# Optimization experiments

Measured on AMD Instinct MI355X. Metric: run time of the kernel, lower is better.

Reference implementation:

```python
import jax, jax.numpy as jnp
import numpy as np

NQ = 12  # num_qubits
NL = 4   # num_layers (StronglyEntanglingLayers depth)
BATCH = 512


def _rx(a):
    # RX(a) = [[cos(a/2), -i sin(a/2)], [-i sin(a/2), cos(a/2)]]; a: (...,) float -> (...,2,2) complex64
    c = jnp.cos(a / 2)
    s = jnp.sin(a / 2)
    return jnp.stack([jnp.stack([c + 0j, -1j * s], -1),
                      jnp.stack([-1j * s, c + 0j], -1)], -2)


def _rot(phi, theta, omega):
    # Pennylane Rot(phi,theta,omega) = RZ(omega) RY(theta) RZ(phi)
    ct = jnp.cos(theta / 2)
    st = jnp.sin(theta / 2)
    ep = jnp.exp(-0.5j * (phi + omega))   # e^{-i(phi+omega)/2}
    em = jnp.exp(-0.5j * (phi - omega))   # e^{-i(phi-omega)/2}
    return jnp.stack([jnp.stack([ep * ct, -jnp.conj(em) * st], -1),
                      jnp.stack([em * st, jnp.conj(ep) * ct], -1)], -2)


def _apply_1q_shared(state, U, q):
    # state: (B,) + (2,)*n; U: (2,2) shared across batch
    s = jnp.moveaxis(state, q + 1, -1)
    s = s @ U.T
    return jnp.moveaxis(s, -1, q + 1)


def _apply_1q_batched(state, U, q):
    # U: (B,2,2), one gate per batch element (AngleEmbedding)
    s = jnp.moveaxis(state, q + 1, -1)
    s = jnp.einsum('b...i,bij->b...j', s, U)
    return jnp.moveaxis(s, -1, q + 1)


def _apply_cnot(state, c, t):
    # flip target axis on the control=1 slice
    s = jnp.moveaxis(state, (c + 1, t + 1), (1, 2))  # (B,2,2,rest)
    s = jnp.stack([s[:, 0], s[:, 1, ::-1]], axis=1)
    return jnp.moveaxis(s, (1, 2), (c + 1, t + 1))


def _circuit(batch_inputs, weights):
    B, n = batch_inputs.shape
    state = jnp.zeros((B, 2 ** n), jnp.complex64).at[:, 0].set(1.0)
    state = state.reshape((B,) + (2,) * n)
    # AngleEmbedding: RX(x_i) on wire i
    Ux = _rx(batch_inputs)  # (B,n,2,2)
    for q in range(n):
        state = _apply_1q_batched(state, Ux[:, q], q)
    # StronglyEntanglingLayers: per layer Rot on each wire then CNOT ring with range r
    Ur = _rot(weights[..., 0], weights[..., 1], weights[..., 2])  # (L,n,2,2)
    for l in range(NL):
        for q in range(n):
            state = _apply_1q_shared(state, Ur[l, q], q)
        r = (l % (n - 1)) + 1  # pennylane default ranges
        for q in range(n):
            state = _apply_cnot(state, q, (q + r) % n)
    # <Z_q> = p(0 on q) - p(1 on q)
    probs = state.real ** 2 + state.imag ** 2
    zs = []
    for q in range(n):
        p = jnp.moveaxis(probs, q + 1, 1).reshape(B, 2, -1).sum(-1)
        zs.append(p[:, 0] - p[:, 1])
    return jnp.stack(zs, axis=1)  # (B,n) float32


def setup_inputs() -> dict:
    key = jax.random.key(0)
    k1, k2, k3, k4 = jax.random.split(key, 4)
    return {
        'batch_inputs': jax.random.normal(k1, (BATCH, NQ), dtype=jnp.float32),
        'weights': jax.random.normal(k2, (NL, NQ, 3), dtype=jnp.float32),
        'head_w': jax.random.normal(k3, (1, NQ), dtype=jnp.float32) / np.sqrt(NQ),
        'head_b': jax.random.normal(k4, (1,), dtype=jnp.float32),
    }


def reference(batch_inputs, weights, head_w, head_b):
    expvals = _circuit(batch_inputs, weights)      # (B, NQ)
    return (expvals @ head_w.T + head_b)[:, 0]     # (B,)
```

## Files before the change

kernel.cpp:

```cpp
#include <hip/hip_runtime.h>

#define NQ 12
#define NL 4
#define NT 256

typedef float f32x2 __attribute__((ext_vector_type(2)));

constexpr unsigned sidx_c(unsigned x) { return x ^ ((x >> 4) & 15u) ^ ((x >> 8) & 15u); }

constexpr unsigned gmap_inv(int l, unsigned v) {
    int r = l + 1; unsigned x = v;
    for (int q = 0; q < NQ; ++q) {
        int cb = NQ - 1 - q, tw = (q + r) % NQ, tb = NQ - 1 - tw;
        x ^= ((x >> cb) & 1u) << tb;
    }
    return x;
}

struct Tabs {
    unsigned lcol[3][8];
    unsigned scol[3][16];
    unsigned rfin[NQ];
};
constexpr Tabs make_tabs() {
    Tabs T{};
    for (int l = 0; l < 3; ++l) {
        unsigned colb[12];
        for (int bit = 0; bit < 12; ++bit) colb[bit] = sidx_c(gmap_inv(l, 1u << bit)) << 3;
        for (int j = 0; j < 6; ++j) T.lcol[l][j] = colb[4 + j];
        T.lcol[l][6] = colb[10];
        T.lcol[l][7] = colb[11];
        for (int s = 0; s < 16; ++s) {
            unsigned v = 0;
            for (int bp = 0; bp < 4; ++bp) if ((s >> bp) & 1) v ^= colb[bp];
            T.scol[l][s] = v;
        }
    }
    for (int q = 0; q < NQ; ++q) {
        const int bpos = 11 - q;
        unsigned m = 0;
        for (int j = 0; j < 12; ++j)
            m |= ((gmap_inv(3, 1u << j) >> bpos) & 1u) << j;
        T.rfin[q] = m;
    }
    return T;
}
__constant__ Tabs TB = make_tabs();
constexpr Tabs CT = make_tabs();

template<int CTRL>
__device__ __forceinline__ f32x2 dpp2(f32x2 v) {
    f32x2 r;
    r.x = __int_as_float(__builtin_amdgcn_update_dpp(__float_as_int(v.x), __float_as_int(v.x), CTRL, 0xF, 0xF, false));
    r.y = __int_as_float(__builtin_amdgcn_update_dpp(__float_as_int(v.y), __float_as_int(v.y), CTRL, 0xF, 0xF, false));
    return r;
}
__device__ __forceinline__ void pswap32(f32x2 v, f32x2& lo, f32x2& hi) {
    float ax = v.x, bx = v.x;
    asm("v_permlane32_swap_b32 %0, %1" : "+v"(ax), "+v"(bx));
    float ay = v.y, by = v.y;
    asm("v_permlane32_swap_b32 %0, %1" : "+v"(ay), "+v"(by));
    lo = f32x2{ax, ay}; hi = f32x2{bx, by};
}
__device__ __forceinline__ void pswap16(f32x2 v, f32x2& ev, f32x2& od) {
    float ax = v.x, bx = v.x;
    asm("v_permlane16_swap_b32 %0, %1" : "+v"(ax), "+v"(bx));
    float ay = v.y, by = v.y;
    asm("v_permlane16_swap_b32 %0, %1" : "+v"(ay), "+v"(by));
    ev = f32x2{ax, ay}; od = f32x2{bx, by};
}

__device__ __forceinline__ void gates2to11(f32x2 rp[8], f32x2 ip[8], const float (*gmL)[8], int lane) {
    {
        const float4 ga = *(const float4*)&gmL[2][0];
        const float4 gb = *(const float4*)&gmL[2][4];
        const int h = (lane >> 5) & 1;
        const float car = h ? gb.x : ga.x, cai = h ? gb.y : ga.y;
        const float cbr = h ? gb.z : ga.z, cbi = h ? gb.w : ga.w;
        #pragma unroll
        for (int k = 0; k < 8; ++k) {
            f32x2 r0r, r1r, r0i, r1i;
            pswap32(rp[k], r0r, r1r);
            pswap32(ip[k], r0i, r1i);
            rp[k] = car*r0r - cai*r0i + cbr*r1r - cbi*r1i;
            ip[k] = cai*r0r + car*r0i + cbi*r1r + cbr*r1i;
        }
    }
    {
        const float4 ga = *(const float4*)&gmL[3][0];
        const float4 gb = *(const float4*)&gmL[3][4];
        const int h = (lane >> 4) & 1;
        const float car = h ? gb.x : ga.x, cai = h ? gb.y : ga.y;
        const float cbr = h ? gb.z : ga.z, cbi = h ? gb.w : ga.w;
        #pragma unroll
        for (int k = 0; k < 8; ++k) {
            f32x2 r0r, r1r, r0i, r1i;
            pswap16(rp[k], r0r, r1r);
            pswap16(ip[k], r0i, r1i);
            rp[k] = car*r0r - cai*r0i + cbr*r1r - cbi*r1i;
            ip[k] = cai*r0r + car*r0i + cbi*r1r + cbr*r1i;
        }
    }
    {
        const float4 ga = *(const float4*)&gmL[4][0];
        const float4 gb = *(const float4*)&gmL[4][4];
        const int h = (lane >> 3) & 1;
        const float cMer = h ? gb.z : ga.x, cMei = h ? gb.w : ga.y;
        const float cOtr = h ? gb.x : ga.z, cOti = h ? gb.y : ga.w;
        #pragma unroll
        for (int k = 0; k < 8; ++k) {
            const f32x2 pR = dpp2<0x128>(rp[k]), pI = dpp2<0x128>(ip[k]);
            const f32x2 nr = cMer*rp[k] - cMei*ip[k] + cOtr*pR - cOti*pI;
            const f32x2 ni = cMei*rp[k] + cMer*ip[k] + cOti*pR + cOtr*pI;
            rp[k] = nr; ip[k] = ni;
        }
    }
    {
        const float4 ga = *(const float4*)&gmL[5][0];
        const float4 gb = *(const float4*)&gmL[5][4];
        const int h = (lane >> 2) & 1;
        const float cMer = h ? gb.z : ga.x, cMei = h ? gb.w : ga.y;
        const float cOtr = h ? gb.x : ga.z, cOti = h ? gb.y : ga.w;
        #pragma unroll
        for (int k = 0; k < 8; ++k) {
            const f32x2 pR = dpp2<0xB1>(dpp2<0x4E>(dpp2<0x141>(rp[k])));
            const f32x2 pI = dpp2<0xB1>(dpp2<0x4E>(dpp2<0x141>(ip[k])));
            const f32x2 nr = cMer*rp[k] - cMei*ip[k] + cOtr*pR - cOti*pI;
            const f32x2 ni = cMei*rp[k] + cMer*ip[k] + cOti*pR + cOtr*pI;
            rp[k] = nr; ip[k] = ni;
        }
    }
    {
        const float4 ga = *(const float4*)&gmL[6][0];
        const float4 gb = *(const float4*)&gmL[6][4];
        const int h = (lane >> 1) & 1;
        const float cMer = h ? gb.z : ga.x, cMei = h ? gb.w : ga.y;
        const float cOtr = h ? gb.x : ga.z, cOti = h ? gb.y : ga.w;
        #pragma unroll
        for (int k = 0; k < 8; ++k) {
            const f32x2 pR = dpp2<0x4E>(rp[k]), pI = dpp2<0x4E>(ip[k]);
            const f32x2 nr = cMer*rp[k] - cMei*ip[k] + cOtr*pR - cOti*pI;
            const f32x2 ni = cMei*rp[k] + cMer*ip[k] + cOti*pR + cOtr*pI;
            rp[k] = nr; ip[k] = ni;
        }
    }
    {
        const float4 ga = *(const float4*)&gmL[7][0];
        const float4 gb = *(const float4*)&gmL[7][4];
        const int h = lane & 1;
        const float cMer = h ? gb.z : ga.x, cMei = h ? gb.w : ga.y;
        const float cOtr = h ? gb.x : ga.z, cOti = h ? gb.y : ga.w;
        #pragma unroll
        for (int k = 0; k < 8; ++k) {
            const f32x2 pR = dpp2<0xB1>(rp[k]), pI = dpp2<0xB1>(ip[k]);
            const f32x2 nr = cMer*rp[k] - cMei*ip[k] + cOtr*pR - cOti*pI;
            const f32x2 ni = cMei*rp[k] + cMer*ip[k] + cOti*pR + cOtr*pI;
            rp[k] = nr; ip[k] = ni;
        }
    }
    #pragma unroll
    for (int wq = 8; wq <= 10; ++wq) {
        const int rb2 = 10 - wq;
        const float4 ga = *(const float4*)&gmL[wq][0];
        const float4 gb = *(const float4*)&gmL[wq][4];
        #pragma unroll
        for (int h2 = 0; h2 < 4; ++h2) {
            const int k0 = ((h2 >> rb2) << (rb2 + 1)) | (h2 & ((1 << rb2) - 1));
            const int k1 = k0 | (1 << rb2);
            const f32x2 a0r = rp[k0], a0i = ip[k0], a1r = rp[k1], a1i = ip[k1];
            rp[k0] = ga.x*a0r - ga.y*a0i + ga.z*a1r - ga.w*a1i;
            ip[k0] = ga.y*a0r + ga.x*a0i + ga.w*a1r + ga.z*a1i;
            rp[k1] = gb.x*a0r - gb.y*a0i + gb.z*a1r - gb.w*a1i;
            ip[k1] = gb.y*a0r + gb.x*a0i + gb.w*a1r + gb.z*a1i;
        }
    }
    {
        const float4 ga = *(const float4*)&gmL[11][0];
        const float4 gb = *(const float4*)&gmL[11][4];
        const f32x2 K0r = f32x2{ga.x, gb.x}, K0i = f32x2{ga.y, gb.y};
        const f32x2 K1r = f32x2{ga.z, gb.z}, K1i = f32x2{ga.w, gb.w};
        #pragma unroll
        for (int k = 0; k < 8; ++k) {
            const float a0r = rp[k].x, a0i = ip[k].x, a1r = rp[k].y, a1i = ip[k].y;
            rp[k] = K0r*a0r - K0i*a0i + K1r*a1r - K1i*a1i;
            ip[k] = K0i*a0r + K0r*a0i + K1i*a1r + K1r*a1i;
        }
    }
}

__device__ __forceinline__ void read_w01(f32x2 rp[8], f32x2 ip[8], const float2* st, unsigned wbyte,
                                         const float (*gmL)[8], int b11, int b10) {
    const float4 ga0 = *(const float4*)&gmL[0][0];
    const float4 gb0 = *(const float4*)&gmL[0][4];
    const float4 ga1 = *(const float4*)&gmL[1][0];
    const float4 gb1 = *(const float4*)&gmL[1][4];
    const float d0r = b11 ? gb0.z : ga0.x, d0i = b11 ? gb0.w : ga0.y;
    const float o0r = b11 ? gb0.x : ga0.z, o0i = b11 ? gb0.y : ga0.w;
    const float d1r = b10 ? gb1.z : ga1.x, d1i = b10 ? gb1.w : ga1.y;
    const float o1r = b10 ? gb1.x : ga1.z, o1i = b10 ? gb1.y : ga1.w;
    const float dwr  = d0r*d1r - d0i*d1i, dwi  = d0r*d1i + d0i*d1r;
    const float dp1r = o0r*d1r - o0i*d1i, dp1i = o0r*d1i + o0i*d1r;
    const float dp2r = d0r*o1r - d0i*o1i, dp2i = d0r*o1i + d0i*o1r;
    const float dp3r = o0r*o1r - o0i*o1i, dp3i = o0r*o1i + o0i*o1r;
    #pragma unroll
    for (int k = 0; k < 8; ++k) {
        const unsigned a0 = wbyte ^ ((unsigned)(2 * k) << 3);
        const unsigned a1 = a0 ^ 8u;
        const float2 o_0 = *(const float2*)((const char*)st + a0);
        const float2 o_1 = *(const float2*)((const char*)st + a1);
        const float2 v_0 = *(const float2*)((const char*)st + (a0 ^ 0x2020u));
        const float2 v_1 = *(const float2*)((const char*)st + (a1 ^ 0x2020u));
        const float2 u_0 = *(const float2*)((const char*)st + (a0 ^ 0x4040u));
        const float2 u_1 = *(const float2*)((const char*)st + (a1 ^ 0x4040u));
        const float2 w_0 = *(const float2*)((const char*)st + (a0 ^ 0x6060u));
        const float2 w_1 = *(const float2*)((const char*)st + (a1 ^ 0x6060u));
        const f32x2 orr = f32x2{o_0.x, o_1.x}, oii = f32x2{o_0.y, o_1.y};
        const f32x2 p2r = f32x2{v_0.x, v_1.x}, p2i = f32x2{v_0.y, v_1.y};
        const f32x2 p1r = f32x2{u_0.x, u_1.x}, p1i = f32x2{u_0.y, u_1.y};
        const f32x2 p3r = f32x2{w_0.x, w_1.x}, p3i = f32x2{w_0.y, w_1.y};
        rp[k] = dwr*orr - dwi*oii + dp1r*p1r - dp1i*p1i + dp2r*p2r - dp2i*p2i + dp3r*p3r - dp3i*p3i;
        ip[k] = dwi*orr + dwr*oii + dp1i*p1r + dp1r*p1i + dp2i*p2r + dp2r*p2i + dp3i*p3r + dp3r*p3i;
    }
}

__device__ __forceinline__ void scatter_l(const f32x2 rp[8], const f32x2 ip[8], float2* st,
                                          int l, int lane, int b10, int b11) {
    unsigned sbase = 0;
    #pragma unroll
    for (int j = 0; j < 6; ++j) if ((lane >> j) & 1) sbase ^= TB.lcol[l][j];
    if (b10) sbase ^= TB.lcol[l][6];
    if (b11) sbase ^= TB.lcol[l][7];
    #pragma unroll
    for (int k = 0; k < 8; ++k) {
        *(float2*)((char*)st + (sbase ^ TB.scol[l][2 * k]))     = make_float2(rp[k].x, ip[k].x);
        *(float2*)((char*)st + (sbase ^ TB.scol[l][2 * k + 1])) = make_float2(rp[k].y, ip[k].y);
    }
}

__global__ __launch_bounds__(NT) void qsim_kernel(
    const float* __restrict__ xin,
    const float* __restrict__ wts,
    const float* __restrict__ hw,
    const float* __restrict__ hb,
    float* __restrict__ out)
{
    __shared__ float2 st[4096];
    __shared__ float  gm[NL * NQ][8];
    __shared__ float  wred[4];

    const int tid  = threadIdx.x;
    const int lane = tid & 63;
    const int wv   = tid >> 6;
    const int b    = blockIdx.x;
    const int b11  = wv >> 1, b10 = wv & 1;

    if (tid < NL * NQ) {
        const float phi = wts[tid * 3 + 0];
        const float th  = wts[tid * 3 + 1];
        const float om  = wts[tid * 3 + 2];
        const float ct  = cosf(0.5f * th), stt = sinf(0.5f * th);
        const float apo = -0.5f * (phi + om), amo = -0.5f * (phi - om);
        const float epr = cosf(apo), epi = sinf(apo);
        const float emr = cosf(amo), emi = sinf(amo);
        float* g = gm[tid];
        g[0] =  epr * ct;  g[1] =  epi * ct;
        g[2] = -emr * stt; g[3] =  emi * stt;
        g[4] =  emr * stt; g[5] =  emi * stt;
        g[6] =  epr * ct;  g[7] = -epi * ct;
    }

    float cv[NQ], sv[NQ];
    #pragma unroll
    for (int bp = 0; bp < NQ; ++bp) {
        const float a = 0.5f * xin[b * NQ + (NQ - 1 - bp)];
        cv[bp] = __cosf(a); sv[bp] = __sinf(a);
    }
    float MS[16];
    MS[0] = cv[0]; MS[1] = sv[0];
    #pragma unroll
    for (int bit = 1; bit < 4; ++bit) {
        #pragma unroll
        for (int j = (1 << bit) - 1; j >= 0; --j) {
            MS[j | (1 << bit)] = MS[j] * sv[bit];
            MS[j]              = MS[j] * cv[bit];
        }
    }

    const unsigned xbase = ((unsigned)wv << 10) | ((unsigned)lane << 4);
    const unsigned wbyte = (xbase ^ ((xbase >> 4) & 15u) ^ ((xbase >> 8) & 15u)) << 3;

    __syncthreads();

    f32x2 rp[8], ip[8];

    {
        const float m00 = cv[11]*cv[10], m01 = cv[11]*sv[10];
        const float m10 = sv[11]*cv[10], m11s = sv[11]*sv[10];
        const float* G0 = gm[0];
        const float* G1 = gm[1];
        const float u0ar = b11 ? G0[4] : G0[0], u0ai = b11 ? G0[5] : G0[1];
        const float u0br = b11 ? G0[6] : G0[2], u0bi = b11 ? G0[7] : G0[3];
        const float u1ar = b10 ? G1[4] : G1[0], u1ai = b10 ? G1[5] : G1[1];
        const float u1br = b10 ? G1[6] : G1[2], u1bi = b10 ? G1[7] : G1[3];
        const float t0r = u0ar*m00 + u0bi*m10;
        const float t0i = u0ai*m00 - u0br*m10;
        const float t1r = u0ai*m01 - u0br*m11s;
        const float t1i = -(u0ar*m01) - u0bi*m11s;
        float Ar = u1ar*t0r - u1ai*t0i + u1br*t1r - u1bi*t1i;
        float Ai = u1ai*t0r + u1ar*t0i + u1bi*t1r + u1br*t1i;
        float mm = 1.f;
        #pragma unroll
        for (int j = 0; j < 6; ++j) mm *= ((lane >> j) & 1) ? sv[4 + j] : cv[4 + j];
        Ar *= mm; Ai *= mm;
        const int pcl = __popc((unsigned)lane) & 3;
        float Br, Bi;
        if      (pcl == 0) { Br =  Ar; Bi =  Ai; }
        else if (pcl == 1) { Br =  Ai; Bi = -Ar; }
        else if (pcl == 2) { Br = -Ar; Bi = -Ai; }
        else               { Br = -Ai; Bi =  Ar; }
        #pragma unroll
        for (int s = 0; s < 16; ++s) {
            const float m = MS[s];
            const int pc = __builtin_popcount((unsigned)s) & 3;
            float ar, ai;
            if      (pc == 0) { ar =  Br*m; ai =  Bi*m; }
            else if (pc == 1) { ar =  Bi*m; ai = -Br*m; }
            else if (pc == 2) { ar = -Br*m; ai = -Bi*m; }
            else              { ar = -Bi*m; ai =  Br*m; }
            if (s & 1) { rp[s >> 1].y = ar; ip[s >> 1].y = ai; }
            else       { rp[s >> 1].x = ar; ip[s >> 1].x = ai; }
        }
        gates2to11(rp, ip, &gm[0], lane);
        scatter_l(rp, ip, st, 0, lane, b10, b11);
    }
    __syncthreads();

    for (int l = 1; l < NL; ++l) {
        read_w01(rp, ip, st, wbyte, &gm[l * NQ], b11, b10);
        gates2to11(rp, ip, &gm[l * NQ], lane);
        if (l < 3) {
            __syncthreads();
            scatter_l(rp, ip, st, l, lane, b10, b11);
            __syncthreads();
        }
    }

    {
        float CS[16];
        #pragma unroll
        for (int s = 0; s < 16; ++s) CS[s] = 0.f;
        #pragma unroll
        for (int q = 0; q < NQ; ++q) {
            const unsigned m = CT.rfin[q];
            const float wq = (__popc(xbase & m) & 1) ? -hw[q] : hw[q];
            #pragma unroll
            for (int s = 0; s < 16; ++s)
                CS[s] += (__builtin_popcount((unsigned)s & m) & 1) ? -wq : wq;
        }
        f32x2 acc = f32x2{0.f, 0.f};
        #pragma unroll
        for (int k = 0; k < 8; ++k) {
            const f32x2 pr = rp[k]*rp[k] + ip[k]*ip[k];
            acc += pr * f32x2{CS[2 * k], CS[2 * k + 1]};
        }
        float sres = acc.x + acc.y;
        #pragma unroll
        for (int off = 32; off >= 1; off >>= 1)
            sres += __shfl_xor(sres, off, 64);
        if ((tid & 63) == 0) wred[wv] = sres;
        __syncthreads();
        if (tid == 0) out[b] = wred[0] + wred[1] + wred[2] + wred[3] + hb[0];
    }
}

extern "C" void kernel_launch(void* const* d_in, const int* in_sizes, int n_in,
                              void* d_out, int out_size, void* d_ws, size_t ws_size,
                              hipStream_t stream) {
    const float* x  = (const float*)d_in[0];
    const float* wt = (const float*)d_in[1];
    const float* hw = (const float*)d_in[2];
    const float* hb = (const float*)d_in[3];
    float* outp = (float*)d_out;
    const int B = in_sizes[0] / NQ;
    qsim_kernel<<<B, NT, 0, stream>>>(x, wt, hw, hb, outp);
}
```

Baseline: 32.55 us.

## Split statevector over 512 threads with three wave-indexed qubits

Doubles the block from 256 to 512 threads so each thread holds 8 amplitudes instead of 16, with qubits 0-2 now mapped to the wave index. The layer-start mixing becomes a three-qubit combine reading 8 partners via float4 LDS loads under a revised swizzle, and the layer loop is unrolled. This is meant to add parallelism and cut per-thread register pressure and latency. In exchange, each amplitude needs more LDS reads per layer and block-wide barriers cover twice as many waves.

```diff
diff --git a/kernel.cpp b/kernel.cpp
--- a/kernel.cpp
+++ b/kernel.cpp
@@ -2,11 +2,11 @@
 
 #define NQ 12
 #define NL 4
-#define NT 256
+#define NT 512
 
 typedef float f32x2 __attribute__((ext_vector_type(2)));
 
-constexpr unsigned sidx_c(unsigned x) { return x ^ ((x >> 4) & 15u) ^ ((x >> 8) & 15u); }
+constexpr unsigned sidx_c(unsigned x) { return x ^ ((x >> 4) & 14u) ^ ((x >> 8) & 14u); }
 
 constexpr unsigned gmap_inv(int l, unsigned v) {
     int r = l + 1; unsigned x = v;
@@ -18,8 +18,8 @@
 }
 
 struct Tabs {
-    unsigned lcol[3][8];
-    unsigned scol[3][16];
+    unsigned lcol[3][9];
+    unsigned scol[3][8];
     unsigned rfin[NQ];
 };
 constexpr Tabs make_tabs() {
@@ -27,12 +27,13 @@
     for (int l = 0; l < 3; ++l) {
         unsigned colb[12];
         for (int bit = 0; bit < 12; ++bit) colb[bit] = sidx_c(gmap_inv(l, 1u << bit)) << 3;
-        for (int j = 0; j < 6; ++j) T.lcol[l][j] = colb[4 + j];
-        T.lcol[l][6] = colb[10];
-        T.lcol[l][7] = colb[11];
-        for (int s = 0; s < 16; ++s) {
+        for (int j = 0; j < 6; ++j) T.lcol[l][j] = colb[3 + j];
+        T.lcol[l][6] = colb[9];
+        T.lcol[l][7] = colb[10];
+        T.lcol[l][8] = colb[11];
+        for (int s = 0; s < 8; ++s) {
             unsigned v = 0;
-            for (int bp = 0; bp < 4; ++bp) if ((s >> bp) & 1) v ^= colb[bp];
+            for (int bp = 0; bp < 3; ++bp) if ((s >> bp) & 1) v ^= colb[bp];
             T.scol[l][s] = v;
         }
     }
@@ -70,15 +71,15 @@
     ev = f32x2{ax, ay}; od = f32x2{bx, by};
 }
 
-__device__ __forceinline__ void gates2to11(f32x2 rp[8], f32x2 ip[8], const float (*gmL)[8], int lane) {
-    {
-        const float4 ga = *(const float4*)&gmL[2][0];
-        const float4 gb = *(const float4*)&gmL[2][4];
+__device__ __forceinline__ void gates3to11(f32x2 rp[4], f32x2 ip[4], const float (*gmL)[8], int lane) {
+    {
+        const float4 ga = *(const float4*)&gmL[3][0];
+        const float4 gb = *(const float4*)&gmL[3][4];
         const int h = (lane >> 5) & 1;
         const float car = h ? gb.x : ga.x, cai = h ? gb.y : ga.y;
         const float cbr = h ? gb.z : ga.z, cbi = h ? gb.w : ga.w;
         #pragma unroll
-        for (int k = 0; k < 8; ++k) {
+        for (int k = 0; k < 4; ++k) {
             f32x2 r0r, r1r, r0i, r1i;
             pswap32(rp[k], r0r, r1r);
             pswap32(ip[k], r0i, r1i);
@@ -87,13 +88,13 @@
         }
     }
     {
-        const float4 ga = *(const float4*)&gmL[3][0];
-        const float4 gb = *(const float4*)&gmL[3][4];
+        const float4 ga = *(const float4*)&gmL[4][0];
+        const float4 gb = *(const float4*)&gmL[4][4];
         const int h = (lane >> 4) & 1;
         const float car = h ? gb.x : ga.x, cai = h ? gb.y : ga.y;
         const float cbr = h ? gb.z : ga.z, cbi = h ? gb.w : ga.w;
         #pragma unroll
-        for (int k = 0; k < 8; ++k) {
+        for (int k = 0; k < 4; ++k) {
             f32x2 r0r, r1r, r0i, r1i;
             pswap16(rp[k], r0r, r1r);
             pswap16(ip[k], r0i, r1i);
@@ -102,13 +103,13 @@
         }
     }
     {
-        const float4 ga = *(const float4*)&gmL[4][0];
-        const float4 gb = *(const float4*)&gmL[4][4];
+        const float4 ga = *(const float4*)&gmL[5][0];
+        const float4 gb = *(const float4*)&gmL[5][4];
         const int h = (lane >> 3) & 1;
         const float cMer = h ? gb.z : ga.x, cMei = h ? gb.w : ga.y;
         const float cOtr = h ? gb.x : ga.z, cOti = h ? gb.y : ga.w;
         #pragma unroll
-        for (int k = 0; k < 8; ++k) {
+        for (int k = 0; k < 4; ++k) {
             const f32x2 pR = dpp2<0x128>(rp[k]), pI = dpp2<0x128>(ip[k]);
             const f32x2 nr = cMer*rp[k] - cMei*ip[k] + cOtr*pR - cOti*pI;
             const f32x2 ni = cMei*rp[k] + cMer*ip[k] + cOti*pR + cOtr*pI;
@@ -116,13 +117,13 @@
         }
     }
     {
-        const float4 ga = *(const float4*)&gmL[5][0];
-        const float4 gb = *(const float4*)&gmL[5][4];
+        const float4 ga = *(const float4*)&gmL[6][0];
+        const float4 gb = *(const float4*)&gmL[6][4];
         const int h = (lane >> 2) & 1;
         const float cMer = h ? gb.z : ga.x, cMei = h ? gb.w : ga.y;
         const float cOtr = h ? gb.x : ga.z, cOti = h ? gb.y : ga.w;
         #pragma unroll
-        for (int k = 0; k < 8; ++k) {
+        for (int k = 0; k < 4; ++k) {
             const f32x2 pR = dpp2<0xB1>(dpp2<0x4E>(dpp2<0x141>(rp[k])));
             const f32x2 pI = dpp2<0xB1>(dpp2<0x4E>(dpp2<0x141>(ip[k])));
             const f32x2 nr = cMer*rp[k] - cMei*ip[k] + cOtr*pR - cOti*pI;
@@ -131,13 +132,13 @@
         }
     }
     {
-        const float4 ga = *(const float4*)&gmL[6][0];
-        const float4 gb = *(const float4*)&gmL[6][4];
+        const float4 ga = *(const float4*)&gmL[7][0];
+        const float4 gb = *(const float4*)&gmL[7][4];
         const int h = (lane >> 1) & 1;
         const float cMer = h ? gb.z : ga.x, cMei = h ? gb.w : ga.y;
         const float cOtr = h ? gb.x : ga.z, cOti = h ? gb.y : ga.w;
         #pragma unroll
-        for (int k = 0; k < 8; ++k) {
+        for (int k = 0; k < 4; ++k) {
             const f32x2 pR = dpp2<0x4E>(rp[k]), pI = dpp2<0x4E>(ip[k]);
             const f32x2 nr = cMer*rp[k] - cMei*ip[k] + cOtr*pR - cOti*pI;
             const f32x2 ni = cMei*rp[k] + cMer*ip[k] + cOti*pR + cOtr*pI;
@@ -145,28 +146,25 @@
         }
     }
     {
-        const float4 ga = *(const float4*)&gmL[7][0];
-        const float4 gb = *(const float4*)&gmL[7][4];
+        const float4 ga = *(const float4*)&gmL[8][0];
+        const float4 gb = *(const float4*)&gmL[8][4];
         const int h = lane & 1;
         const float cMer = h ? gb.z : ga.x, cMei = h ? gb.w : ga.y;
         const float cOtr = h ? gb.x : ga.z, cOti = h ? gb.y : ga.w;
         #pragma unroll
-        for (int k = 0; k < 8; ++k) {
+        for (int k = 0; k < 4; ++k) {
             const f32x2 pR = dpp2<0xB1>(rp[k]), pI = dpp2<0xB1>(ip[k]);
             const f32x2 nr = cMer*rp[k] - cMei*ip[k] + cOtr*pR - cOti*pI;
             const f32x2 ni = cMei*rp[k] + cMer*ip[k] + cOti*pR + cOtr*pI;
             rp[k] = nr; ip[k] = ni;
         }
     }
-    #pragma unroll
-    for (int wq = 8; wq <= 10; ++wq) {
-        const int rb2 = 10 - wq;
-        const float4 ga = *(const float4*)&gmL[wq][0];
-        const float4 gb = *(const float4*)&gmL[wq][4];
-        #pragma unroll
-        for (int h2 = 0; h2 < 4; ++h2) {
-            const int k0 = ((h2 >> rb2) << (rb2 + 1)) | (h2 & ((1 << rb2) - 1));
-            const int k1 = k0 | (1 << rb2);
+    {
+        const float4 ga = *(const float4*)&gmL[9][0];
+        const float4 gb = *(const float4*)&gmL[9][4];
+        #pragma unroll
+        for (int h2 = 0; h2 < 2; ++h2) {
+            const int k0 = h2, k1 = h2 + 2;
             const f32x2 a0r = rp[k0], a0i = ip[k0], a1r = rp[k1], a1i = ip[k1];
             rp[k0] = ga.x*a0r - ga.y*a0i + ga.z*a1r - ga.w*a1i;
             ip[k0] = ga.y*a0r + ga.x*a0i + ga.w*a1r + ga.z*a1i;
@@ -175,12 +173,25 @@
         }
     }
     {
+        const float4 ga = *(const float4*)&gmL[10][0];
+        const float4 gb = *(const float4*)&gmL[10][4];
+        #pragma unroll
+        for (int h2 = 0; h2 < 2; ++h2) {
+            const int k0 = 2 * h2, k1 = k0 + 1;
+            const f32x2 a0r = rp[k0], a0i = ip[k0], a1r = rp[k1], a1i = ip[k1];
+            rp[k0] = ga.x*a0r - ga.y*a0i + ga.z*a1r - ga.w*a1i;
+            ip[k0] = ga.y*a0r + ga.x*a0i + ga.w*a1r + ga.z*a1i;
+            rp[k1] = gb.x*a0r - gb.y*a0i + gb.z*a1r - gb.w*a1i;
+            ip[k1] = gb.y*a0r + gb.x*a0i + gb.w*a1r + gb.z*a1i;
+        }
+    }
+    {
         const float4 ga = *(const float4*)&gmL[11][0];
         const float4 gb = *(const float4*)&gmL[11][4];
         const f32x2 K0r = f32x2{ga.x, gb.x}, K0i = f32x2{ga.y, gb.y};
         const f32x2 K1r = f32x2{ga.z, gb.z}, K1i = f32x2{ga.w, gb.w};
         #pragma unroll
-        for (int k = 0; k < 8; ++k) {
+        for (int k = 0; k < 4; ++k) {
             const float a0r = rp[k].x, a0i = ip[k].x, a1r = rp[k].y, a1i = ip[k].y;
             rp[k] = K0r*a0r - K0i*a0i + K1r*a1r - K1i*a1i;
             ip[k] = K0i*a0r + K0r*a0i + K1i*a1r + K1r*a1i;
@@ -188,50 +199,55 @@
     }
 }
 
-__device__ __forceinline__ void read_w01(f32x2 rp[8], f32x2 ip[8], const float2* st, unsigned wbyte,
-                                         const float (*gmL)[8], int b11, int b10) {
-    const float4 ga0 = *(const float4*)&gmL[0][0];
-    const float4 gb0 = *(const float4*)&gmL[0][4];
-    const float4 ga1 = *(const float4*)&gmL[1][0];
-    const float4 gb1 = *(const float4*)&gmL[1][4];
-    const float d0r = b11 ? gb0.z : ga0.x, d0i = b11 ? gb0.w : ga0.y;
-    const float o0r = b11 ? gb0.x : ga0.z, o0i = b11 ? gb0.y : ga0.w;
-    const float d1r = b10 ? gb1.z : ga1.x, d1i = b10 ? gb1.w : ga1.y;
-    const float o1r = b10 ? gb1.x : ga1.z, o1i = b10 ? gb1.y : ga1.w;
-    const float dwr  = d0r*d1r - d0i*d1i, dwi  = d0r*d1i + d0i*d1r;
-    const float dp1r = o0r*d1r - o0i*d1i, dp1i = o0r*d1i + o0i*d1r;
-    const float dp2r = d0r*o1r - d0i*o1i, dp2i = d0r*o1i + d0i*o1r;
-    const float dp3r = o0r*o1r - o0i*o1i, dp3i = o0r*o1i + o0i*o1r;
-    #pragma unroll
-    for (int k = 0; k < 8; ++k) {
-        const unsigned a0 = wbyte ^ ((unsigned)(2 * k) << 3);
-        const unsigned a1 = a0 ^ 8u;
-        const float2 o_0 = *(const float2*)((const char*)st + a0);
-        const float2 o_1 = *(const float2*)((const char*)st + a1);
-        const float2 v_0 = *(const float2*)((const char*)st + (a0 ^ 0x2020u));
-        const float2 v_1 = *(const float2*)((const char*)st + (a1 ^ 0x2020u));
-        const float2 u_0 = *(const float2*)((const char*)st + (a0 ^ 0x4040u));
-        const float2 u_1 = *(const float2*)((const char*)st + (a1 ^ 0x4040u));
-        const float2 w_0 = *(const float2*)((const char*)st + (a0 ^ 0x6060u));
-        const float2 w_1 = *(const float2*)((const char*)st + (a1 ^ 0x6060u));
-        const f32x2 orr = f32x2{o_0.x, o_1.x}, oii = f32x2{o_0.y, o_1.y};
-        const f32x2 p2r = f32x2{v_0.x, v_1.x}, p2i = f32x2{v_0.y, v_1.y};
-        const f32x2 p1r = f32x2{u_0.x, u_1.x}, p1i = f32x2{u_0.y, u_1.y};
-        const f32x2 p3r = f32x2{w_0.x, w_1.x}, p3i = f32x2{w_0.y, w_1.y};
-        rp[k] = dwr*orr - dwi*oii + dp1r*p1r - dp1i*p1i + dp2r*p2r - dp2i*p2i + dp3r*p3r - dp3i*p3i;
-        ip[k] = dwi*orr + dwr*oii + dp1i*p1r + dp1r*p1i + dp2i*p2r + dp2r*p2i + dp3i*p3r + dp3r*p3i;
-    }
-}
-
-__device__ __forceinline__ void scatter_l(const f32x2 rp[8], const f32x2 ip[8], float2* st,
-                                          int l, int lane, int b10, int b11) {
+__device__ __forceinline__ void read_w012(f32x2 rp[4], f32x2 ip[4], const float2* st, unsigned wbyte,
+                                          const float (*gmL)[8], int b11, int b10, int b9) {
+    const float* G0 = gmL[0];
+    const float* G1 = gmL[1];
+    const float* G2 = gmL[2];
+    const float a0r = G0[6*b11],   a0i = G0[6*b11+1];
+    const float q0r = G0[2*b11+2], q0i = G0[2*b11+3];
+    const float a1r = G1[6*b10],   a1i = G1[6*b10+1];
+    const float q1r = G1[2*b10+2], q1i = G1[2*b10+3];
+    const float a2r = G2[6*b9],    a2i = G2[6*b9+1];
+    const float q2r = G2[2*b9+2],  q2i = G2[2*b9+3];
+    const float m00r = a0r*a1r - a0i*a1i, m00i = a0r*a1i + a0i*a1r;
+    const float m01r = a0r*q1r - a0i*q1i, m01i = a0r*q1i + a0i*q1r;
+    const float m10r = q0r*a1r - q0i*a1i, m10i = q0r*a1i + q0i*a1r;
+    const float m11r = q0r*q1r - q0i*q1i, m11i = q0r*q1i + q0i*q1r;
+    float cr[8], ci[8];
+    cr[0] = m00r*a2r - m00i*a2i; ci[0] = m00r*a2i + m00i*a2r;
+    cr[1] = m00r*q2r - m00i*q2i; ci[1] = m00r*q2i + m00i*q2r;
+    cr[2] = m01r*a2r - m01i*a2i; ci[2] = m01r*a2i + m01i*a2r;
+    cr[3] = m01r*q2r - m01i*q2i; ci[3] = m01r*q2i + m01i*q2r;
+    cr[4] = m10r*a2r - m10i*a2i; ci[4] = m10r*a2i + m10i*a2r;
+    cr[5] = m10r*q2r - m10i*q2i; ci[5] = m10r*q2i + m10i*q2r;
+    cr[6] = m11r*a2r - m11i*a2i; ci[6] = m11r*a2i + m11i*a2r;
+    cr[7] = m11r*q2r - m11i*q2i; ci[7] = m11r*q2i + m11i*q2r;
+    #pragma unroll
+    for (int k = 0; k < 4; ++k) {
+        const unsigned base = wbyte ^ ((unsigned)k << 4);
+        f32x2 rr = f32x2{0.f, 0.f}, ii = f32x2{0.f, 0.f};
+        #pragma unroll
+        for (int o = 0; o < 8; ++o) {
+            const float4 v = *(const float4*)((const char*)st + (base ^ ((unsigned)o * 0x1010u)));
+            const f32x2 sr = f32x2{v.x, v.z}, si = f32x2{v.y, v.w};
+            rr += cr[o]*sr - ci[o]*si;
+            ii += ci[o]*sr + cr[o]*si;
+        }
+        rp[k] = rr; ip[k] = ii;
+    }
+}
+
+__device__ __forceinline__ void scatter_l(const f32x2 rp[4], const f32x2 ip[4], float2* st,
+                                          int l, int lane, int b9, int b10, int b11) {
     unsigned sbase = 0;
     #pragma unroll
     for (int j = 0; j < 6; ++j) if ((lane >> j) & 1) sbase ^= TB.lcol[l][j];
-    if (b10) sbase ^= TB.lcol[l][6];
-    if (b11) sbase ^= TB.lcol[l][7];
-    #pragma unroll
-    for (int k = 0; k < 8; ++k) {
+    if (b9)  sbase ^= TB.lcol[l][6];
+    if (b10) sbase ^= TB.lcol[l][7];
+    if (b11) sbase ^= TB.lcol[l][8];
+    #pragma unroll
+    for (int k = 0; k < 4; ++k) {
         *(float2*)((char*)st + (sbase ^ TB.scol[l][2 * k]))     = make_float2(rp[k].x, ip[k].x);
         *(float2*)((char*)st + (sbase ^ TB.scol[l][2 * k + 1])) = make_float2(rp[k].y, ip[k].y);
     }
@@ -244,15 +260,15 @@
     const float* __restrict__ hb,
     float* __restrict__ out)
 {
-    __shared__ float2 st[4096];
-    __shared__ float  gm[NL * NQ][8];
-    __shared__ float  wred[4];
+    __shared__ alignas(16) float2 st[4096];
+    __shared__ float gm[NL * NQ][8];
+    __shared__ float wred[8];
 
     const int tid  = threadIdx.x;
     const int lane = tid & 63;
     const int wv   = tid >> 6;
     const int b    = blockIdx.x;
-    const int b11  = wv >> 1, b10 = wv & 1;
+    const int b11 = wv >> 2, b10 = (wv >> 1) & 1, b9 = wv & 1;
 
     if (tid < NL * NQ) {
         const float phi = wts[tid * 3 + 0];
@@ -275,10 +291,10 @@
         const float a = 0.5f * xin[b * NQ + (NQ - 1 - bp)];
         cv[bp] = __cosf(a); sv[bp] = __sinf(a);
     }
-    float MS[16];
+    float MS[8];
     MS[0] = cv[0]; MS[1] = sv[0];
     #pragma unroll
-    for (int bit = 1; bit < 4; ++bit) {
+    for (int bit = 1; bit < 3; ++bit) {
         #pragma unroll
         for (int j = (1 << bit) - 1; j >= 0; --j) {
             MS[j | (1 << bit)] = MS[j] * sv[bit];
@@ -286,31 +302,29 @@
         }
     }
 
-    const unsigned xbase = ((unsigned)wv << 10) | ((unsigned)lane << 4);
-    const unsigned wbyte = (xbase ^ ((xbase >> 4) & 15u) ^ ((xbase >> 8) & 15u)) << 3;
+    const unsigned xb = ((unsigned)wv << 9) | ((unsigned)lane << 3);
+    const unsigned wbyte = (xb ^ ((xb >> 4) & 14u) ^ ((xb >> 8) & 14u)) << 3;
 
     __syncthreads();
 
-    f32x2 rp[8], ip[8];
-
-    {
-        const float m00 = cv[11]*cv[10], m01 = cv[11]*sv[10];
-        const float m10 = sv[11]*cv[10], m11s = sv[11]*sv[10];
+    f32x2 rp[4], ip[4];
+
+    {
         const float* G0 = gm[0];
         const float* G1 = gm[1];
-        const float u0ar = b11 ? G0[4] : G0[0], u0ai = b11 ? G0[5] : G0[1];
-        const float u0br = b11 ? G0[6] : G0[2], u0bi = b11 ? G0[7] : G0[3];
-        const float u1ar = b10 ? G1[4] : G1[0], u1ai = b10 ? G1[5] : G1[1];
-        const float u1br = b10 ? G1[6] : G1[2], u1bi = b10 ? G1[7] : G1[3];
-        const float t0r = u0ar*m00 + u0bi*m10;
-        const float t0i = u0ai*m00 - u0br*m10;
-        const float t1r = u0ai*m01 - u0br*m11s;
-        const float t1i = -(u0ar*m01) - u0bi*m11s;
-        float Ar = u1ar*t0r - u1ai*t0i + u1br*t1r - u1bi*t1i;
-        float Ai = u1ai*t0r + u1ar*t0i + u1bi*t1r + u1br*t1i;
+        const float* G2 = gm[2];
+        const float w0r = G0[4*b11]*cv[11]   + G0[4*b11+3]*sv[11];
+        const float w0i = G0[4*b11+1]*cv[11] - G0[4*b11+2]*sv[11];
+        const float w1r = G1[4*b10]*cv[10]   + G1[4*b10+3]*sv[10];
+        const float w1i = G1[4*b10+1]*cv[10] - G1[4*b10+2]*sv[10];
+        const float w2r = G2[4*b9]*cv[9]     + G2[4*b9+3]*sv[9];
+        const float w2i = G2[4*b9+1]*cv[9]   - G2[4*b9+2]*sv[9];
+        const float t01r = w0r*w1r - w0i*w1i, t01i = w0r*w1i + w0i*w1r;
+        float Ar = t01r*w2r - t01i*w2i;
+        float Ai = t01r*w2i + t01i*w2r;
         float mm = 1.f;
         #pragma unroll
-        for (int j = 0; j < 6; ++j) mm *= ((lane >> j) & 1) ? sv[4 + j] : cv[4 + j];
+        for (int j = 0; j < 6; ++j) mm *= ((lane >> j) & 1) ? sv[3 + j] : cv[3 + j];
         Ar *= mm; Ai *= mm;
         const int pcl = __popc((unsigned)lane) & 3;
         float Br, Bi;
@@ -319,7 +333,7 @@
         else if (pcl == 2) { Br = -Ar; Bi = -Ai; }
         else               { Br = -Ai; Bi =  Ar; }
         #pragma unroll
-        for (int s = 0; s < 16; ++s) {
+        for (int s = 0; s < 8; ++s) {
             const float m = MS[s];
             const int pc = __builtin_popcount((unsigned)s) & 3;
             float ar, ai;
@@ -330,36 +344,37 @@
             if (s & 1) { rp[s >> 1].y = ar; ip[s >> 1].y = ai; }
             else       { rp[s >> 1].x = ar; ip[s >> 1].x = ai; }
         }
-        gates2to11(rp, ip, &gm[0], lane);
-        scatter_l(rp, ip, st, 0, lane, b10, b11);
+        gates3to11(rp, ip, &gm[0], lane);
+        scatter_l(rp, ip, st, 0, lane, b9, b10, b11);
     }
     __syncthreads();
 
+    #pragma unroll
     for (int l = 1; l < NL; ++l) {
-        read_w01(rp, ip, st, wbyte, &gm[l * NQ], b11, b10);
-        gates2to11(rp, ip, &gm[l * NQ], lane);
+        read_w012(rp, ip, st, wbyte, &gm[l * NQ], b11, b10, b9);
+        gates3to11(rp, ip, &gm[l * NQ], lane);
         if (l < 3) {
             __syncthreads();
-            scatter_l(rp, ip, st, l, lane, b10, b11);
+            scatter_l(rp, ip, st, l, lane, b9, b10, b11);
             __syncthreads();
         }
     }
 
     {
-        float CS[16];
-        #pragma unroll
-        for (int s = 0; s < 16; ++s) CS[s] = 0.f;
+        float CS[8];
+        #pragma unroll
+        for (int s = 0; s < 8; ++s) CS[s] = 0.f;
         #pragma unroll
         for (int q = 0; q < NQ; ++q) {
             const unsigned m = CT.rfin[q];
-            const float wq = (__popc(xbase & m) & 1) ? -hw[q] : hw[q];
+            const float wq = (__popc(xb & m) & 1) ? -hw[q] : hw[q];
             #pragma unroll
-            for (int s = 0; s < 16; ++s)
+            for (int s = 0; s < 8; ++s)
                 CS[s] += (__builtin_popcount((unsigned)s & m) & 1) ? -wq : wq;
         }
         f32x2 acc = f32x2{0.f, 0.f};
         #pragma unroll
-        for (int k = 0; k < 8; ++k) {
+        for (int k = 0; k < 4; ++k) {
             const f32x2 pr = rp[k]*rp[k] + ip[k]*ip[k];
             acc += pr * f32x2{CS[2 * k], CS[2 * k + 1]};
         }
@@ -367,9 +382,14 @@
         #pragma unroll
         for (int off = 32; off >= 1; off >>= 1)
             sres += __shfl_xor(sres, off, 64);
-        if ((tid & 63) == 0) wred[wv] = sres;
+        if (lane == 0) wred[wv] = sres;
         __syncthreads();
-        if (tid == 0) out[b] = wred[0] + wred[1] + wred[2] + wred[3] + hb[0];
+        if (tid == 0) {
+            float s = hb[0];
+            #pragma unroll
+            for (int w = 0; w < 8; ++w) s += wred[w];
+            out[b] = s;
+        }
     }
 }
 
```

Measured after the change: 35.16 us. +8.0%, slower.
